# Kernel tuning notes

Hardware: AMD Instinct MI355X
Metric: run time of the kernel (lower is better)

Reference implementation:

```python
import jax, jax.numpy as jnp
import numpy as np
from jax import lax

DRUG_LEN = 150
PROT_LEN = 1000
CHAR_DIM = 64
CONV = 40
C4 = CONV * 4  # 160
PROT_OUT = PROT_LEN - (4 - 1) - (8 - 1) - (12 - 1)  # 979


def conv1d(x, w, b):
    # x: (B, Cin, L), w: (Cout, Cin, K) -> (B, Cout, L-K+1), VALID
    y = lax.conv_general_dilated(x, w, window_strides=(1,), padding='VALID',
                                 dimension_numbers=('NCH', 'OIH', 'NCH'))
    return y + b[None, :, None]


def setup_inputs() -> dict:
    key = jax.random.key(0)
    ks = jax.random.split(key, 24)
    B = 4
    drug = jax.random.normal(ks[0], (B, DRUG_LEN, C4), dtype=jnp.float32)
    num_atoms = jax.random.randint(ks[1], (B,), 1, DRUG_LEN + 1)
    protein = jax.random.randint(ks[2], (B, PROT_LEN), 0, 26)

    def lin(k, dout, din, scale=None):
        s = scale if scale is not None else 1.0 / np.sqrt(din)
        kw, kb = jax.random.split(k)
        W = jax.random.uniform(kw, (dout, din), jnp.float32, -s, s)
        b = jax.random.uniform(kb, (dout,), jnp.float32, -s, s)
        return W, b

    protein_embed = jax.random.normal(ks[3], (26, CHAR_DIM), dtype=jnp.float32)
    protein_embed = protein_embed.at[0].set(0.0)  # padding_idx=0

    def conv_w(k, cout, cin, ksz):
        s = 1.0 / np.sqrt(cin * ksz)
        kw, kb = jax.random.split(k)
        w = jax.random.uniform(kw, (cout, cin, ksz), jnp.float32, -s, s)
        b = jax.random.uniform(kb, (cout,), jnp.float32, -s, s)
        return w, b

    w1, b1 = conv_w(ks[4], CONV, CHAR_DIM, 4)
    w2, b2 = conv_w(ks[5], CONV * 2, CONV, 8)
    w3, b3 = conv_w(ks[6], C4, CONV * 2, 12)
    Wd, bd = lin(ks[7], C4, C4)
    Wp, bp = lin(ks[8], C4, C4)
    Watt, batt = lin(ks[9], C4, C4)
    W1, bf1 = lin(ks[10], 1024, C4 * 2)
    W2, bf2 = lin(ks[11], 1024, 1024)
    W3, bf3 = lin(ks[12], 512, 1024)
    Wo, bo = lin(ks[13], 2, 512)
    return dict(drug=drug, num_atoms=num_atoms, protein=protein,
                protein_embed=protein_embed, w1=w1, b1=b1, w2=w2, b2=b2,
                w3=w3, b3=b3, Wd=Wd, bd=bd, Wp=Wp, bp=bp, Watt=Watt,
                batt=batt, W1=W1, bf1=bf1, W2=W2, bf2=bf2, W3=W3, bf3=bf3,
                Wo=Wo, bo=bo)


def _forward(drug, num_atoms, protein, protein_embed, w1, b1, w2, b2, w3, b3,
             Wd, bd, Wp, bp, Watt, batt, W1, bf1, W2, bf2, W3, bf3, Wo, bo):
    relu = jax.nn.relu
    drugConv = jnp.transpose(drug, (0, 2, 1))                 # (B,160,150)
    pe = jnp.transpose(protein_embed[protein], (0, 2, 1))     # (B,64,1000)
    h = relu(conv1d(pe, w1, b1))
    h = relu(conv1d(h, w2, b2))
    proteinConv = relu(conv1d(h, w3, b3))                     # (B,160,979)

    drug_att = drug @ Wd.T + bd                               # (B,150,160)
    dmask = (jnp.arange(DRUG_LEN)[None, :] < num_atoms[:, None])
    drug_att = drug_att * dmask[:, :, None]
    protein_att = jnp.transpose(proteinConv, (0, 2, 1)) @ Wp.T + bp  # (B,979,160)
    pmask = (protein > 0)[:, :PROT_OUT]
    protein_att = protein_att * pmask[:, :, None]

    # Broadcast outer-sum + relu; Linear commutes with mean (affine), so apply
    # attention_layer after reducing, identical math to Linear-then-mean.
    R = relu(drug_att[:, :, None, :] + protein_att[:, None, :, :])  # (B,150,979,160)
    Cmean = jnp.mean(R, axis=2)  # (B,150,160)
    Pmean = jnp.mean(R, axis=1)  # (B,979,160)
    Compound_atte = jax.nn.sigmoid(Cmean @ Watt.T + batt)  # (B,150,160)
    Protein_atte = jax.nn.sigmoid(Pmean @ Watt.T + batt)   # (B,979,160)

    drugConv = drugConv * (0.5 + jnp.transpose(Compound_atte, (0, 2, 1)))
    proteinConv = proteinConv * (0.5 + jnp.transpose(Protein_atte, (0, 2, 1)))
    d = jnp.max(drugConv, axis=2)      # (B,160) max-pool over full length
    p = jnp.max(proteinConv, axis=2)   # (B,160)
    pair = jnp.concatenate([d, p], axis=1)  # (B,320)

    lrelu = lambda x: jax.nn.leaky_relu(x, 0.01)
    f1 = lrelu(pair @ W1.T + bf1)
    f2 = lrelu(f1 @ W2.T + bf2)
    f3 = lrelu(f2 @ W3.T + bf3)
    return f3 @ Wo.T + bo  # (B,2)


def reference(drug, num_atoms, protein, protein_embed, w1, b1, w2, b2, w3, b3,
              Wd, bd, Wp, bp, Watt, batt, W1, bf1, W2, bf2, W3, bf3, Wo, bo):
    return _forward(drug, num_atoms, protein, protein_embed, w1, b1, w2, b2,
                    w3, b3, Wd, bd, Wp, bp, Watt, batt, W1, bf1, W2, bf2,
                    W3, bf3, Wo, bo)
```

## Files before the change

kernel.cpp:

```cpp
#include <hip/hip_runtime.h>
#include <math.h>

#define BB 4
#define DL 150
#define PL 1000
#define CD 64
#define NC1 40
#define NC2 80
#define NC3 160
#define L1O 997
#define L2O 990
#define L3O 979
#define L3P 980
#define DLP 152
#define PLP 984
#define JP 992
#define NINF (-1e30f)

typedef __attribute__((ext_vector_type(8))) short bf16x8;
typedef __attribute__((ext_vector_type(4))) float f32x4;

__device__ __forceinline__ float relu_(float x){ return fmaxf(x, 0.f); }
__device__ __forceinline__ float lrelu_(float x){ return x > 0.f ? x : 0.01f * x; }

__device__ __forceinline__ unsigned fenc(float x){
  unsigned u = __float_as_uint(x);
  return (u & 0x80000000u) ? ~u : (u | 0x80000000u);
}
__device__ __forceinline__ float fdec(unsigned u){
  return __uint_as_float((u & 0x80000000u) ? (u & 0x7fffffffu) : ~u);
}
__device__ __forceinline__ unsigned short bf16_(float x){
  unsigned u = __float_as_uint(x);
  unsigned r = (u + 0x7FFFu + ((u >> 16) & 1u)) >> 16;
  return (unsigned short)r;
}

__device__ __forceinline__ f32x4 mfma_k160(const unsigned short* __restrict__ Wb,
                                           const unsigned short* __restrict__ Xb,
                                           int co0, int j0, int lane){
  int col = lane & 15, g = lane >> 4;
  f32x4 acc = {0.f, 0.f, 0.f, 0.f};
  const unsigned short* wr = Wb + (size_t)(co0 + col) * 160 + g * 8;
  const unsigned short* xr = Xb + (size_t)(j0 + col) * 160 + g * 8;
  #pragma unroll
  for (int k0 = 0; k0 < 5; k0++){
    bf16x8 av = *(const bf16x8*)(wr + k0 * 32);
    bf16x8 bv = *(const bf16x8*)(xr + k0 * 32);
    acc = __builtin_amdgcn_mfma_f32_16x16x32_bf16(av, bv, acc, 0, 0, 0);
  }
  return acc;
}

__global__ __launch_bounds__(256) void k_prep(const float* __restrict__ emb,
                       const float* __restrict__ w1, float* __restrict__ projG,
                       const float* __restrict__ w3, unsigned short* __restrict__ w3r,
                       const float* __restrict__ Wp, unsigned short* __restrict__ Wpb,
                       const float* __restrict__ Watt, unsigned short* __restrict__ Wattb,
                       const float* __restrict__ Wd, unsigned short* __restrict__ Wdb,
                       const float* __restrict__ w2, unsigned short* __restrict__ w2r,
                       const float* __restrict__ drug, unsigned short* __restrict__ drugb){
  int blk = blockIdx.x;
  if (blk < 17){
    int e = blk * 256 + threadIdx.x;
    if (e >= 26 * 160) return;
    int tok = e / 160, rem = e % 160, k = rem / 40, co = rem % 40;
    float a = 0.f;
    const float* er = emb + tok * CD;
    const float* wr = w1 + co * (CD * 4) + k;
    #pragma unroll 8
    for (int ci = 0; ci < CD; ci++) a = fmaf(er[ci], wr[ci * 4], a);
    projG[tok * 161 + k * 40 + co] = a;
    return;
  }
  if (blk < 737){
    int e = (blk - 17) * 256 + threadIdx.x;
    int kk = e / (160 * 96); int r = e % (160 * 96);
    int co = r / 96, ci = r % 96;
    float v = (ci < NC2) ? w3[(size_t)co * 960 + ci * 12 + kk] : 0.f;
    w3r[e] = bf16_(v);
    return;
  }
  if (blk < 837){
    int e = (blk - 737) * 256 + threadIdx.x;
    Wpb[e] = bf16_(Wp[e]);
    return;
  }
  if (blk < 937){
    int e = (blk - 837) * 256 + threadIdx.x;
    Wattb[e] = bf16_(Watt[e]);
    return;
  }
  if (blk < 1037){
    int e = (blk - 937) * 256 + threadIdx.x;
    Wdb[e] = bf16_(Wd[e]);
    return;
  }
  if (blk < 1197){
    int e = (blk - 1037) * 256 + threadIdx.x;
    int kk = e / (80 * 64); int r = e % (80 * 64);
    int co = r / 64, ci = r % 64;
    float v = (ci < NC1) ? w2[(size_t)(co * NC1 + ci) * 8 + kk] : 0.f;
    w2r[e] = bf16_(v);
    return;
  }
  {
    int e = (blk - 1197) * 256 + threadIdx.x;
    int b = e / 25600; int r = e % 25600;
    int i = r / 160, c = r % 160;
    float v = (i < DL) ? drug[((size_t)b * DL + i) * 160 + c] : 0.f;
    drugb[e] = bf16_(v);
  }
}

__global__ __launch_bounds__(256) void k_conv1(const int* __restrict__ prot,
                        const float* __restrict__ projG, const float* __restrict__ b1,
                        unsigned short* __restrict__ h1bT){
  __shared__ float sp[26 * 161];
  int b = blockIdx.x / 125;
  int t = (blockIdx.x % 125) * 256 + threadIdx.x;
  for (int k = threadIdx.x; k < 26 * 161; k += 256) sp[k] = projG[k];
  __syncthreads();
  int ci = (t & 31) * 2, p = t >> 5;
  float v0 = 0.f, v1 = 0.f;
  if (p < L1O && ci < NC1){
    const int* pr = prot + b * PL + p;
    int t0 = pr[0], t1 = pr[1], t2 = pr[2], t3 = pr[3];
    v0 = relu_(b1[ci] + sp[t0 * 161 + ci] + sp[t1 * 161 + 40 + ci]
             + sp[t2 * 161 + 80 + ci] + sp[t3 * 161 + 120 + ci]);
    int c1 = ci + 1;
    v1 = relu_(b1[c1] + sp[t0 * 161 + c1] + sp[t1 * 161 + 40 + c1]
             + sp[t2 * 161 + 80 + c1] + sp[t3 * 161 + 120 + c1]);
  }
  ushort2 o; o.x = bf16_(v0); o.y = bf16_(v1);
  *(ushort2*)(&h1bT[((size_t)b * 1000 + p) * 64 + ci]) = o;
}

__global__ __launch_bounds__(256) void k_c2m(const unsigned short* __restrict__ h1bT,
                        const unsigned short* __restrict__ w2r,
                        const float* __restrict__ bias,
                        unsigned short* __restrict__ h2bT){
  int blk = blockIdx.x;
  int pt = blk % 16; int t = blk / 16;
  int cog = t % 5; int b = t / 5;
  int co0 = cog * 16;
  int wave = threadIdx.x >> 6, lane = threadIdx.x & 63;
  int col = lane & 15, g = lane >> 4;
  int p0 = pt * 64 + wave * 16;
  if (p0 >= JP) return;
  f32x4 acc = {0.f, 0.f, 0.f, 0.f};
  const unsigned short* wbase = w2r + (size_t)(co0 + col) * 64 + g * 8;
  const unsigned short* xbase = h1bT + (size_t)b * 1000 * 64 + g * 8;
  int prow = p0 + col;
  #pragma unroll 2
  for (int kk = 0; kk < 8; kk++){
    int rp = prow + kk; if (rp > 999) rp = 999;
    const unsigned short* xr = xbase + (size_t)rp * 64;
    const unsigned short* wr = wbase + (size_t)kk * (80 * 64);
    #pragma unroll
    for (int ks = 0; ks < 2; ks++){
      bf16x8 av = *(const bf16x8*)(wr + ks * 32);
      bf16x8 bv = *(const bf16x8*)(xr + ks * 32);
      acc = __builtin_amdgcn_mfma_f32_16x16x32_bf16(av, bv, acc, 0, 0, 0);
    }
  }
  int p = p0 + col;
  if (p < JP){
    unsigned short tb[4];
    bool live = p < L2O;
    #pragma unroll
    for (int r = 0; r < 4; r++){
      int co = co0 + g * 4 + r;
      tb[r] = live ? bf16_(relu_(acc[r] + bias[co])) : (unsigned short)0;
    }
    *(uint2*)(&h2bT[((size_t)b * JP + p) * 96 + co0 + g * 4]) = *(uint2*)tb;
    if (cog == 4){
      uint2 z = {0u, 0u};
      *(uint2*)(&h2bT[((size_t)b * JP + p) * 96 + 80 + g * 4]) = z;
    }
  }
}

__global__ __launch_bounds__(256) void k_c3m(const unsigned short* __restrict__ h2bT,
                        const unsigned short* __restrict__ w3r,
                        const float* __restrict__ bias, float* __restrict__ pconv,
                        unsigned short* __restrict__ pconvTb){
  int blk = blockIdx.x;
  int pt = blk % 16; int t = blk / 16;
  int cog = t % 10; int b = t / 10;
  int co0 = cog * 16;
  int wave = threadIdx.x >> 6, lane = threadIdx.x & 63;
  int col = lane & 15, g = lane >> 4;
  int p0 = pt * 64 + wave * 16;
  f32x4 acc = {0.f, 0.f, 0.f, 0.f};
  const unsigned short* wbase = w3r + (size_t)(co0 + col) * 96 + g * 8;
  const unsigned short* xbase = h2bT + (size_t)b * JP * 96 + g * 8;
  int prow = p0 + col;
  for (int kk = 0; kk < 12; kk++){
    int rp = prow + kk; if (rp > 991) rp = 991;
    const unsigned short* xr = xbase + (size_t)rp * 96;
    const unsigned short* wr = wbase + (size_t)kk * (160 * 96);
    #pragma unroll
    for (int ks = 0; ks < 3; ks++){
      bf16x8 av = *(const bf16x8*)(wr + ks * 32);
      bf16x8 bv = *(const bf16x8*)(xr + ks * 32);
      acc = __builtin_amdgcn_mfma_f32_16x16x32_bf16(av, bv, acc, 0, 0, 0);
    }
  }
  if (p0 >= L3O) return;
  int p = p0 + col;
  if (p < L3O){
    unsigned short tb[4];
    #pragma unroll
    for (int r = 0; r < 4; r++){
      int co = co0 + g * 4 + r;
      float v = acc[r] + bias[co];
      pconv[(size_t)(b * NC3 + co) * L3P + p] = v;
      tb[r] = bf16_(relu_(v));
    }
    *(uint2*)(&pconvTb[((size_t)b * JP + p) * 160 + co0 + g * 4]) = *(uint2*)tb;
  }
}

__global__ __launch_bounds__(256) void k_pattm(const unsigned short* __restrict__ drugb,
                        const int* __restrict__ natoms,
                        const unsigned short* __restrict__ Wdb,
                        const float* __restrict__ bd,
                        float* __restrict__ dattT, unsigned* __restrict__ enc,
                        const unsigned short* __restrict__ pconvTb,
                        const int* __restrict__ prot,
                        const unsigned short* __restrict__ Wpb,
                        const float* __restrict__ bp, float* __restrict__ pattT){
  int blk = blockIdx.x;
  int tid = threadIdx.x;
  int wave = tid >> 6, lane = tid & 63;
  int col = lane & 15, g = lane >> 4;
  if (blk < 40){
    if (blk == 0){
      for (int k = tid; k < 2 * BB * NC3; k += 256) enc[k] = 0u;
    }
    int b = blk / 10, it = blk % 10;
    int i0 = it * 16;
    const unsigned short* Xb = drugb + (size_t)b * 160 * 160;
    for (int ct = wave; ct < 10; ct += 4){
      int co0 = ct * 16;
      f32x4 acc = mfma_k160(Wdb, Xb, co0, i0, lane);
      int i = i0 + col;
      if (i < DL){
        bool act = i < natoms[b];
        #pragma unroll
        for (int r = 0; r < 4; r++){
          int co = co0 + g * 4 + r;
          dattT[(size_t)(b * NC3 + co) * DLP + i] = act ? (acc[r] + bd[co]) : 0.f;
        }
      }
    }
    return;
  }
  int q = blk - 40;
  int jt = q % 62, b = q / 62;
  int j0 = jt * 16;
  const unsigned short* Xb = pconvTb + (size_t)b * JP * 160;
  for (int ct = wave; ct < 10; ct += 4){
    int co0 = ct * 16;
    f32x4 acc = mfma_k160(Wpb, Xb, co0, j0, lane);
    int j = j0 + col;
    if (j < L3O){
      bool act = prot[b * PL + j] > 0;
      #pragma unroll
      for (int r = 0; r < 4; r++){
        int co = co0 + g * 4 + r;
        pattT[(size_t)(b * NC3 + co) * PLP + j] = act ? (acc[r] + bp[co]) : 0.f;
      }
    }
  }
}

__global__ __launch_bounds__(256) void k_means(const float* __restrict__ dattT,
                        const float* __restrict__ pattT,
                        unsigned short* __restrict__ cmeanTb,
                        unsigned short* __restrict__ pmeanTb){
  __shared__ __align__(16) float sda[DLP];
  __shared__ __align__(16) float spa[PLP];
  __shared__ float scm[4][DLP];
  int b = blockIdx.x / NC3, c = blockIdx.x % NC3;
  int tid = threadIdx.x;
  const float4* dr = (const float4*)(dattT + (size_t)(b * NC3 + c) * DLP);
  const float4* pr = (const float4*)(pattT + (size_t)(b * NC3 + c) * PLP);
  if (tid < DLP / 4) *(float4*)(&sda[tid * 4]) = dr[tid];
  if (tid < PLP / 4) *(float4*)(&spa[tid * 4]) = pr[tid];
  __syncthreads();
  for (int t = tid; t < 600; t += 256){
    int i = t >> 2, qq = t & 3;
    int js = qq * 244;
    int je = (qq == 3) ? L3O : js + 244;
    float v = sda[i];
    float s0 = 0.f, s1 = 0.f, s2 = 0.f, s3 = 0.f;
    const float4* p4 = (const float4*)(spa + js);
    int n4 = (je - js) >> 2;
    for (int u = 0; u < n4; u++){
      float4 p = p4[u];
      s0 += relu_(v + p.x); s1 += relu_(v + p.y);
      s2 += relu_(v + p.z); s3 += relu_(v + p.w);
    }
    for (int j = js + n4 * 4; j < je; j++) s0 += relu_(v + spa[j]);
    scm[qq][i] = (s0 + s1) + (s2 + s3);
  }
  for (int j = tid; j < L3O; j += 256){
    float v = spa[j];
    float s0 = 0.f, s1 = 0.f, s2 = 0.f, s3 = 0.f;
    const float4* d4 = (const float4*)sda;
    #pragma unroll 4
    for (int u = 0; u < 37; u++){
      float4 d = d4[u];
      s0 += relu_(v + d.x); s1 += relu_(v + d.y);
      s2 += relu_(v + d.z); s3 += relu_(v + d.w);
    }
    s0 += relu_(v + sda[148]); s1 += relu_(v + sda[149]);
    float pm = ((s0 + s1) + (s2 + s3)) * (1.f / DL);
    pmeanTb[((size_t)b * JP + j) * 160 + c] = bf16_(pm);
  }
  __syncthreads();
  if (tid < 160){
    float s = 0.f;
    if (tid < DL)
      s = ((scm[0][tid] + scm[1][tid]) + (scm[2][tid] + scm[3][tid])) * (1.f / L3O);
    cmeanTb[((size_t)b * 160 + tid) * 160 + c] = bf16_(s);
  }
}

__global__ __launch_bounds__(256) void k_attem(const unsigned short* __restrict__ cmeanTb,
                        const unsigned short* __restrict__ pmeanTb,
                        const unsigned short* __restrict__ Wattb,
                        const float* __restrict__ batt,
                        const float* __restrict__ drug,
                        const float* __restrict__ pconv, unsigned* __restrict__ enc){
  int blk = blockIdx.x;
  int tid = threadIdx.x;
  int wave = tid >> 6, lane = tid & 63;
  int col = lane & 15, g = lane >> 4;
  if (blk < 40){
    int b = blk / 10, cot = blk % 10;
    int co0 = cot * 16;
    const unsigned short* Xb = cmeanTb + (size_t)b * 160 * 160;
    float m[4];
    #pragma unroll
    for (int r = 0; r < 4; r++) m[r] = NINF;
    for (int it = wave; it < 10; it += 4){
      int i0 = it * 16;
      f32x4 acc = mfma_k160(Wattb, Xb, co0, i0, lane);
      int i = i0 + col;
      if (i < DL){
        #pragma unroll
        for (int r = 0; r < 4; r++){
          int co = co0 + g * 4 + r;
          float gate = 1.f / (1.f + expf(-(acc[r] + batt[co])));
          float val = drug[((size_t)b * DL + i) * 160 + co] * (0.5f + gate);
          m[r] = fmaxf(m[r], val);
        }
      }
    }
    #pragma unroll
    for (int r = 0; r < 4; r++){
      #pragma unroll
      for (int off = 1; off < 16; off <<= 1)
        m[r] = fmaxf(m[r], __shfl_xor(m[r], off, 64));
    }
    if (col == 0){
      #pragma unroll
      for (int r = 0; r < 4; r++)
        atomicMax(&enc[b * NC3 + co0 + g * 4 + r], fenc(m[r]));
    }
    return;
  }
  int q = blk - 40;
  int jt = q % 62, b = q / 62;
  int j0 = jt * 16;
  const unsigned short* Xb = pmeanTb + (size_t)b * JP * 160;
  for (int ct = wave; ct < 10; ct += 4){
    int co0 = ct * 16;
    f32x4 acc = mfma_k160(Wattb, Xb, co0, j0, lane);
    int j = j0 + col;
    float m[4];
    #pragma unroll
    for (int r = 0; r < 4; r++){
      int co = co0 + g * 4 + r;
      if (j < L3O){
        float gate = 1.f / (1.f + expf(-(acc[r] + batt[co])));
        float pv = relu_(pconv[(size_t)(b * NC3 + co) * L3P + j]);
        m[r] = pv * (0.5f + gate);
      } else m[r] = NINF;
    }
    #pragma unroll
    for (int r = 0; r < 4; r++){
      #pragma unroll
      for (int off = 1; off < 16; off <<= 1)
        m[r] = fmaxf(m[r], __shfl_xor(m[r], off, 64));
    }
    if (col == 0){
      #pragma unroll
      for (int r = 0; r < 4; r++)
        atomicMax(&enc[BB * NC3 + b * NC3 + co0 + g * 4 + r], fenc(m[r]));
    }
  }
}

__global__ __launch_bounds__(256) void k_mlp1(const unsigned* __restrict__ enc,
                        const float* __restrict__ W1, const float* __restrict__ bf1,
                        float* __restrict__ f1){
  int b = blockIdx.x >> 6, og = blockIdx.x & 63;
  int o = og * 16 + (threadIdx.x >> 4);
  int q = threadIdx.x & 15;
  const float4* wr = (const float4*)(W1 + (size_t)o * 320);
  float4 a = make_float4(0.f, 0.f, 0.f, 0.f);
  #pragma unroll
  for (int mi = 0; mi < 5; mi++){
    int k4 = q + mi * 16;
    int k = k4 * 4;
    const unsigned* e = (k < 160) ? (enc + b * NC3 + k)
                                  : (enc + BB * NC3 + b * NC3 + (k - 160));
    float4 wv = wr[k4];
    a.x = fmaf(fdec(e[0]), wv.x, a.x);
    a.y = fmaf(fdec(e[1]), wv.y, a.y);
    a.z = fmaf(fdec(e[2]), wv.z, a.z);
    a.w = fmaf(fdec(e[3]), wv.w, a.w);
  }
  float r = a.x + a.y + a.z + a.w;
  r += __shfl_xor(r, 1, 64); r += __shfl_xor(r, 2, 64);
  r += __shfl_xor(r, 4, 64); r += __shfl_xor(r, 8, 64);
  if (q == 0) f1[b * 1024 + o] = lrelu_(r + bf1[o]);
}

__global__ __launch_bounds__(256) void k_mlp2(const float* __restrict__ x,
                        const float* __restrict__ W, const float* __restrict__ bias,
                        float* __restrict__ y){
  int b = blockIdx.x >> 6, og = blockIdx.x & 63;
  int o = og * 16 + (threadIdx.x >> 4);
  int q = threadIdx.x & 15;
  const float4* wr = (const float4*)(W + (size_t)o * 1024);
  const float4* xr = (const float4*)(x + b * 1024);
  float4 a = make_float4(0.f, 0.f, 0.f, 0.f);
  #pragma unroll
  for (int mi = 0; mi < 16; mi++){
    int k4 = q + mi * 16;
    float4 wv = wr[k4], xv = xr[k4];
    a.x = fmaf(xv.x, wv.x, a.x);
    a.y = fmaf(xv.y, wv.y, a.y);
    a.z = fmaf(xv.z, wv.z, a.z);
    a.w = fmaf(xv.w, wv.w, a.w);
  }
  float r = a.x + a.y + a.z + a.w;
  r += __shfl_xor(r, 1, 64); r += __shfl_xor(r, 2, 64);
  r += __shfl_xor(r, 4, 64); r += __shfl_xor(r, 8, 64);
  if (q == 0) y[b * 1024 + o] = lrelu_(r + bias[o]);
}

__global__ __launch_bounds__(256) void k_mlp3(const float* __restrict__ x,
                        const float* __restrict__ W, const float* __restrict__ bias,
                        float* __restrict__ y){
  int b = blockIdx.x >> 5, og = blockIdx.x & 31;
  int o = og * 16 + (threadIdx.x >> 4);
  int q = threadIdx.x & 15;
  const float4* wr = (const float4*)(W + (size_t)o * 1024);
  const float4* xr = (const float4*)(x + b * 1024);
  float4 a = make_float4(0.f, 0.f, 0.f, 0.f);
  #pragma unroll
  for (int mi = 0; mi < 16; mi++){
    int k4 = q + mi * 16;
    float4 wv = wr[k4], xv = xr[k4];
    a.x = fmaf(xv.x, wv.x, a.x);
    a.y = fmaf(xv.y, wv.y, a.y);
    a.z = fmaf(xv.z, wv.z, a.z);
    a.w = fmaf(xv.w, wv.w, a.w);
  }
  float r = a.x + a.y + a.z + a.w;
  r += __shfl_xor(r, 1, 64); r += __shfl_xor(r, 2, 64);
  r += __shfl_xor(r, 4, 64); r += __shfl_xor(r, 8, 64);
  if (q == 0) y[b * 512 + o] = lrelu_(r + bias[o]);
}

__global__ void k_mlp4(const float* __restrict__ f3, const float* __restrict__ Wo,
                       const float* __restrict__ bo, float* __restrict__ out){
  int tid = threadIdx.x;
  int g = tid >> 5, lane = tid & 31;
  int b = g >> 1, o = g & 1;
  const float4* xr = (const float4*)(f3 + b * 512);
  const float4* wr = (const float4*)(Wo + o * 512);
  float4 a = make_float4(0.f, 0.f, 0.f, 0.f);
  #pragma unroll
  for (int mI = 0; mI < 4; mI++){
    int k4 = lane + mI * 32;
    float4 xv = xr[k4], wv = wr[k4];
    a.x = fmaf(xv.x, wv.x, a.x);
    a.y = fmaf(xv.y, wv.y, a.y);
    a.z = fmaf(xv.z, wv.z, a.z);
    a.w = fmaf(xv.w, wv.w, a.w);
  }
  float r = a.x + a.y + a.z + a.w;
  for (int off = 16; off; off >>= 1) r += __shfl_xor(r, off, 64);
  if (lane == 0) out[b * 2 + o] = r + bo[o];
}

extern "C" void kernel_launch(void* const* d_in, const int* in_sizes, int n_in,
                              void* d_out, int out_size, void* d_ws, size_t ws_size,
                              hipStream_t stream) {
  const float* drug  = (const float*)d_in[0];
  const int*   natoms= (const int*)d_in[1];
  const int*   prot  = (const int*)d_in[2];
  const float* emb   = (const float*)d_in[3];
  const float* w1    = (const float*)d_in[4];
  const float* b1    = (const float*)d_in[5];
  const float* w2    = (const float*)d_in[6];
  const float* b2    = (const float*)d_in[7];
  const float* w3    = (const float*)d_in[8];
  const float* b3    = (const float*)d_in[9];
  const float* Wd    = (const float*)d_in[10];
  const float* bd    = (const float*)d_in[11];
  const float* Wp    = (const float*)d_in[12];
  const float* bp    = (const float*)d_in[13];
  const float* Watt  = (const float*)d_in[14];
  const float* batt  = (const float*)d_in[15];
  const float* W1    = (const float*)d_in[16];
  const float* bf1   = (const float*)d_in[17];
  const float* W2    = (const float*)d_in[18];
  const float* bf2   = (const float*)d_in[19];
  const float* W3    = (const float*)d_in[20];
  const float* bf3   = (const float*)d_in[21];
  const float* Wo    = (const float*)d_in[22];
  const float* bo    = (const float*)d_in[23];
  float* out = (float*)d_out;

  float* ws = (float*)d_ws;
  float* f1     = ws;
  float* f2     = ws + 4096;
  float* f3     = ws + 8192;
  float* dattT  = ws + 10240;
  float* pattT  = ws + 107520;
  float* pconv  = ws + 737280;
  unsigned* enc = (unsigned*)(ws + 1364480);
  float* projG  = ws + 1364864;
  unsigned short* h1bT    = (unsigned short*)(ws + 1369088);
  unsigned short* w2r     = (unsigned short*)(ws + 1497088);
  unsigned short* h2bT    = (unsigned short*)(ws + 1517568);
  unsigned short* w3r     = (unsigned short*)(ws + 1708032);
  unsigned short* pconvTb = (unsigned short*)(ws + 1800192);
  unsigned short* pmeanTb = (unsigned short*)(ws + 2117632);
  unsigned short* cmeanTb = (unsigned short*)(ws + 2435072);
  unsigned short* drugb   = (unsigned short*)(ws + 2486272);
  unsigned short* Wpb     = (unsigned short*)(ws + 2537472);
  unsigned short* Wattb   = (unsigned short*)(ws + 2550272);
  unsigned short* Wdb     = (unsigned short*)(ws + 2563072);

  k_prep  <<<1597, 256, 0, stream>>>(emb, w1, projG, w3, w3r, Wp, Wpb,
                                     Watt, Wattb, Wd, Wdb, w2, w2r, drug, drugb);
  k_conv1 <<<500, 256, 0, stream>>>(prot, projG, b1, h1bT);
  k_c2m   <<<320, 256, 0, stream>>>(h1bT, w2r, b2, h2bT);
  k_c3m   <<<640, 256, 0, stream>>>(h2bT, w3r, b3, pconv, pconvTb);
  k_pattm <<<288, 256, 0, stream>>>(drugb, natoms, Wdb, bd, dattT, enc,
                                    pconvTb, prot, Wpb, bp, pattT);
  k_means <<<BB * NC3, 256, 0, stream>>>(dattT, pattT, cmeanTb, pmeanTb);
  k_attem <<<288, 256, 0, stream>>>(cmeanTb, pmeanTb, Wattb, batt, drug,
                                    pconv, enc);
  k_mlp1  <<<256, 256, 0, stream>>>(enc, W1, bf1, f1);
  k_mlp2  <<<256, 256, 0, stream>>>(f1, W2, bf2, f2);
  k_mlp3  <<<128, 256, 0, stream>>>(f2, W3, bf3, f3);
  k_mlp4  <<<1, 256, 0, stream>>>(f3, Wo, bo, out);
}
```

Measured before the change: 98.47 us.

## Fuse conv2 and conv3 via shared-memory halo tile of conv2 output

Merges the conv2 and conv3 kernels into one. Each block recomputes an 80-row halo tile of the conv2 output (all 80 channels) into LDS, then runs the conv3 MFMA loop from shared memory instead of a global h2bT buffer. This removes one launch and the global round trip of the intermediate activation. In exchange, conv2 is recomputed redundantly across the 10 output-channel groups and the 64-row tiles, and the kernel now uses LDS.

```diff
diff --git a/kernel.cpp b/kernel.cpp
--- a/kernel.cpp
+++ b/kernel.cpp
@@ -15,6 +15,7 @@
 #define DLP 152
 #define PLP 984
 #define JP 992
+#define H2W 104
 #define NINF (-1e30f)
 
 typedef __attribute__((ext_vector_type(8))) short bf16x8;
@@ -136,69 +137,64 @@
   *(ushort2*)(&h1bT[((size_t)b * 1000 + p) * 64 + ci]) = o;
 }
 
-__global__ __launch_bounds__(256) void k_c2m(const unsigned short* __restrict__ h1bT,
+__global__ __launch_bounds__(256) void k_c23m(const unsigned short* __restrict__ h1bT,
                         const unsigned short* __restrict__ w2r,
-                        const float* __restrict__ bias,
-                        unsigned short* __restrict__ h2bT){
-  int blk = blockIdx.x;
-  int pt = blk % 16; int t = blk / 16;
-  int cog = t % 5; int b = t / 5;
-  int co0 = cog * 16;
-  int wave = threadIdx.x >> 6, lane = threadIdx.x & 63;
-  int col = lane & 15, g = lane >> 4;
-  int p0 = pt * 64 + wave * 16;
-  if (p0 >= JP) return;
-  f32x4 acc = {0.f, 0.f, 0.f, 0.f};
-  const unsigned short* wbase = w2r + (size_t)(co0 + col) * 64 + g * 8;
-  const unsigned short* xbase = h1bT + (size_t)b * 1000 * 64 + g * 8;
-  int prow = p0 + col;
-  #pragma unroll 2
-  for (int kk = 0; kk < 8; kk++){
-    int rp = prow + kk; if (rp > 999) rp = 999;
-    const unsigned short* xr = xbase + (size_t)rp * 64;
-    const unsigned short* wr = wbase + (size_t)kk * (80 * 64);
-    #pragma unroll
-    for (int ks = 0; ks < 2; ks++){
-      bf16x8 av = *(const bf16x8*)(wr + ks * 32);
-      bf16x8 bv = *(const bf16x8*)(xr + ks * 32);
-      acc = __builtin_amdgcn_mfma_f32_16x16x32_bf16(av, bv, acc, 0, 0, 0);
-    }
-  }
-  int p = p0 + col;
-  if (p < JP){
-    unsigned short tb[4];
-    bool live = p < L2O;
-    #pragma unroll
-    for (int r = 0; r < 4; r++){
-      int co = co0 + g * 4 + r;
-      tb[r] = live ? bf16_(relu_(acc[r] + bias[co])) : (unsigned short)0;
-    }
-    *(uint2*)(&h2bT[((size_t)b * JP + p) * 96 + co0 + g * 4]) = *(uint2*)tb;
-    if (cog == 4){
-      uint2 z = {0u, 0u};
-      *(uint2*)(&h2bT[((size_t)b * JP + p) * 96 + 80 + g * 4]) = z;
-    }
-  }
-}
-
-__global__ __launch_bounds__(256) void k_c3m(const unsigned short* __restrict__ h2bT,
+                        const float* __restrict__ b2,
                         const unsigned short* __restrict__ w3r,
-                        const float* __restrict__ bias, float* __restrict__ pconv,
+                        const float* __restrict__ b3,
+                        float* __restrict__ pconv,
                         unsigned short* __restrict__ pconvTb){
+  __shared__ unsigned short h2t[80 * H2W];
   int blk = blockIdx.x;
   int pt = blk % 16; int t = blk / 16;
   int cog = t % 10; int b = t / 10;
+  int tid = threadIdx.x;
+  int wave = tid >> 6, lane = tid & 63;
+  int col = lane & 15, g = lane >> 4;
+  int ptbase = pt * 64;
+  for (int i = tid; i < 640; i += 256){
+    int r = i >> 3, c = i & 7;
+    *(unsigned*)(&h2t[r * H2W + 80 + c * 2]) = 0u;
+  }
+  for (int tp = wave; tp < 25; tp += 4){
+    int psub = tp / 5, cot = tp % 5;
+    int co0 = cot * 16;
+    int p0 = ptbase + psub * 16;
+    f32x4 acc = {0.f, 0.f, 0.f, 0.f};
+    const unsigned short* wbase = w2r + (size_t)(co0 + col) * 64 + g * 8;
+    const unsigned short* xbase = h1bT + (size_t)b * 1000 * 64 + g * 8;
+    int prow = p0 + col;
+    #pragma unroll 2
+    for (int kk = 0; kk < 8; kk++){
+      int rp = prow + kk; if (rp > 999) rp = 999;
+      const unsigned short* xr = xbase + (size_t)rp * 64;
+      const unsigned short* wr = wbase + (size_t)kk * (80 * 64);
+      #pragma unroll
+      for (int ks = 0; ks < 2; ks++){
+        bf16x8 av = *(const bf16x8*)(wr + ks * 32);
+        bf16x8 bv = *(const bf16x8*)(xr + ks * 32);
+        acc = __builtin_amdgcn_mfma_f32_16x16x32_bf16(av, bv, acc, 0, 0, 0);
+      }
+    }
+    int p = p0 + col;
+    bool live = p < L2O;
+    unsigned short tb[4];
+    #pragma unroll
+    for (int r = 0; r < 4; r++){
+      int co = co0 + g * 4 + r;
+      tb[r] = live ? bf16_(relu_(acc[r] + b2[co])) : (unsigned short)0;
+    }
+    int rl = psub * 16 + col;
+    *(uint2*)(&h2t[rl * H2W + co0 + g * 4]) = *(uint2*)tb;
+  }
+  __syncthreads();
+  f32x4 acc = {0.f, 0.f, 0.f, 0.f};
   int co0 = cog * 16;
-  int wave = threadIdx.x >> 6, lane = threadIdx.x & 63;
-  int col = lane & 15, g = lane >> 4;
-  int p0 = pt * 64 + wave * 16;
-  f32x4 acc = {0.f, 0.f, 0.f, 0.f};
   const unsigned short* wbase = w3r + (size_t)(co0 + col) * 96 + g * 8;
-  const unsigned short* xbase = h2bT + (size_t)b * JP * 96 + g * 8;
-  int prow = p0 + col;
+  int rl0 = wave * 16 + col;
   for (int kk = 0; kk < 12; kk++){
-    int rp = prow + kk; if (rp > 991) rp = 991;
-    const unsigned short* xr = xbase + (size_t)rp * 96;
+    int rl = rl0 + kk;
+    const unsigned short* xr = &h2t[rl * H2W + g * 8];
     const unsigned short* wr = wbase + (size_t)kk * (160 * 96);
     #pragma unroll
     for (int ks = 0; ks < 3; ks++){
@@ -207,14 +203,13 @@
       acc = __builtin_amdgcn_mfma_f32_16x16x32_bf16(av, bv, acc, 0, 0, 0);
     }
   }
-  if (p0 >= L3O) return;
-  int p = p0 + col;
+  int p = ptbase + wave * 16 + col;
   if (p < L3O){
     unsigned short tb[4];
     #pragma unroll
     for (int r = 0; r < 4; r++){
       int co = co0 + g * 4 + r;
-      float v = acc[r] + bias[co];
+      float v = acc[r] + b3[co];
       pconv[(size_t)(b * NC3 + co) * L3P + p] = v;
       tb[r] = bf16_(relu_(v));
     }
@@ -541,7 +536,6 @@
   float* projG  = ws + 1364864;
   unsigned short* h1bT    = (unsigned short*)(ws + 1369088);
   unsigned short* w2r     = (unsigned short*)(ws + 1497088);
-  unsigned short* h2bT    = (unsigned short*)(ws + 1517568);
   unsigned short* w3r     = (unsigned short*)(ws + 1708032);
   unsigned short* pconvTb = (unsigned short*)(ws + 1800192);
   unsigned short* pmeanTb = (unsigned short*)(ws + 2117632);
@@ -554,8 +548,7 @@
   k_prep  <<<1597, 256, 0, stream>>>(emb, w1, projG, w3, w3r, Wp, Wpb,
                                      Watt, Wattb, Wd, Wdb, w2, w2r, drug, drugb);
   k_conv1 <<<500, 256, 0, stream>>>(prot, projG, b1, h1bT);
-  k_c2m   <<<320, 256, 0, stream>>>(h1bT, w2r, b2, h2bT);
-  k_c3m   <<<640, 256, 0, stream>>>(h2bT, w3r, b3, pconv, pconvTb);
+  k_c23m  <<<640, 256, 0, stream>>>(h1bT, w2r, b2, w3r, b3, pconv, pconvTb);
   k_pattm <<<288, 256, 0, stream>>>(drugb, natoms, Wdb, bd, dattT, enc,
                                     pconvTb, prot, Wpb, bp, pattT);
   k_means <<<BB * NC3, 256, 0, stream>>>(dattT, pattT, cmeanTb, pmeanTb);
```

Result: slower. 150.4 us (+52.7%).
